# Kernel tuning notes

Hardware: AMD Instinct MI355X
Metric: run time of the kernel (lower is better)

Reference implementation:

```python
import jax, jax.numpy as jnp
import numpy as np

N_NODES = 50000
N_EDGES = 800000
D_IN = 128
HID = 128
N_CLASSES = 2
N_GRAPHS = 500
N_LAYERS = 7


def setup_inputs() -> dict:
    key = jax.random.key(0)
    ks = jax.random.split(key, 8)
    x = jax.random.normal(ks[0], (N_NODES, D_IN), dtype=jnp.float32)
    edge_index = jax.random.randint(ks[1], (2, N_EDGES), 0, N_NODES, dtype=jnp.int32)
    batch = jnp.sort(jax.random.randint(ks[2], (N_NODES,), 0, N_GRAPHS, dtype=jnp.int32))
    s = 1.0 / np.sqrt(HID).astype(np.float32)
    # SAGEConv params: Wl (neighbor lin, with bias bl), Wr (root lin, no bias)
    Wl = jax.random.normal(ks[3], (N_LAYERS, HID, HID), dtype=jnp.float32) * s
    Wr = jax.random.normal(ks[4], (N_LAYERS, HID, HID), dtype=jnp.float32) * s
    bl = jnp.zeros((N_LAYERS, HID), dtype=jnp.float32)
    W_out = jax.random.normal(ks[5], (HID, N_CLASSES), dtype=jnp.float32) * s
    b_out = jnp.zeros((N_CLASSES,), dtype=jnp.float32)
    return {"x": x, "edge_index": edge_index, "batch": batch,
            "Wl": Wl, "Wr": Wr, "bl": bl, "W_out": W_out, "b_out": b_out}


def reference(x, edge_index, batch, Wl, Wr, bl, W_out, b_out):
    n = x.shape[0]
    src, dst = edge_index[0], edge_index[1]  # messages flow src -> dst
    deg = jax.ops.segment_sum(jnp.ones_like(dst, dtype=x.dtype), dst, num_segments=n)
    inv_deg = (1.0 / jnp.clip(deg, 1.0))[:, None]  # [N,1]; zero-degree -> aggregate stays 0

    def sage_layer(h, i):
        # mean aggregation of neighbor features, then linear + root linear
        agg = jax.ops.segment_sum(h[src], dst, num_segments=n) * inv_deg  # [N,H]
        return agg @ Wl[i] + bl[i] + h @ Wr[i]

    h = x
    for i in range(N_LAYERS - 1):
        h = jax.nn.relu(sage_layer(h, i))
    h = sage_layer(h, N_LAYERS - 1)  # last conv: no relu

    pooled = jax.ops.segment_sum(h, batch, num_segments=N_GRAPHS)  # global_add_pool
    # F.dropout with training=False is identity (eval mode)
    return pooled @ W_out + b_out  # [G, num_classes]
```

## Files before the change

### kernel.cpp

```cpp
#include <hip/hip_runtime.h>
#include <stdint.h>

#define NN 50000
#define NE 800000
#define HID 128
#define NG 500
#define NL 7

typedef short bf16x8 __attribute__((ext_vector_type(8)));
typedef float f32x4 __attribute__((ext_vector_type(4)));

__device__ __forceinline__ unsigned short f2bf(float f) {
  unsigned int u = __builtin_bit_cast(unsigned int, f);
  u += 0x7FFFu + ((u >> 16) & 1u);
  return (unsigned short)(u >> 16);
}
__device__ __forceinline__ float bf2f(unsigned short h) {
  unsigned int u = ((unsigned int)h) << 16;
  return __builtin_bit_cast(float, u);
}
__device__ __forceinline__ float bflo(unsigned int u) {
  return __builtin_bit_cast(float, u << 16);
}
__device__ __forceinline__ float bfhi(unsigned int u) {
  return __builtin_bit_cast(float, u & 0xffff0000u);
}

__global__ void k_pre(const float* __restrict__ x, unsigned short* __restrict__ hA,
                      unsigned short* __restrict__ hB,
                      const int* __restrict__ dstE, int* __restrict__ deg,
                      const float* __restrict__ Wl, const float* __restrict__ Wr,
                      unsigned short* __restrict__ wswh,
                      unsigned short* __restrict__ wswl) {
  int i = blockIdx.x * 256 + threadIdx.x;
  if (i < NN * HID / 4) {
    float4 v = ((const float4*)x)[i];
    ushort4 r;
    r.x = f2bf(v.x); r.y = f2bf(v.y); r.z = f2bf(v.z); r.w = f2bf(v.w);
    ((ushort4*)hA)[i] = r;
  }
  if (i < NE) atomicAdd(&deg[dstE[i]], 1);
  if (i < NL * 2 * 4 * 4096) {
    int j = i & 7, ii = (i >> 3) & 15, q = (i >> 7) & 3, t = (i >> 9) & 7;
    int cc = (i >> 12) & 3, m = (i >> 14) & 1, l = i >> 15;
    int k = cc * 32 + q * 8 + j, n = t * 16 + ii;
    const float* W = m ? Wr : Wl;
    float w = W[l * HID * HID + k * HID + n];
    unsigned short hi = f2bf(w);
    unsigned short lo = f2bf(w - bf2f(hi));
    wswh[i] = hi;
    wswl[i] = lo;
  }
  if (i < 2048) {
    int b = i >> 10, r = (i >> 4) & 63, u = i & 15;
    unsigned short* pad = (b ? hB : hA) + (size_t)(NN + r) * HID;
    *(uint4*)&pad[u * 8] = make_uint4(0u, 0u, 0u, 0u);
  }
}

__global__ void k_scan1(const int* __restrict__ deg, int* __restrict__ offs,
                        int* __restrict__ bsum) {
  int i = blockIdx.x * 256 + threadIdx.x;
  int v = (i < NN) ? deg[i] : 0;
  int lane = threadIdx.x & 63, wv = threadIdx.x >> 6;
  int x = v;
  #pragma unroll
  for (int d = 1; d < 64; d <<= 1) {
    int y = __shfl_up(x, d, 64);
    if (lane >= d) x += y;
  }
  __shared__ int wsum[4];
  if (lane == 63) wsum[wv] = x;
  __syncthreads();
  if (threadIdx.x == 0) {
    int s = 0;
    for (int k = 0; k < 4; k++) { int t = wsum[k]; wsum[k] = s; s += t; }
    bsum[blockIdx.x] = s;
  }
  __syncthreads();
  if (i < NN) offs[i] = x - v + wsum[wv];
}

__global__ void k_scan2(int* __restrict__ bsum, int nb) {
  int i = threadIdx.x;
  int v = (i < nb) ? bsum[i] : 0;
  int lane = threadIdx.x & 63, wv = threadIdx.x >> 6;
  int x = v;
  #pragma unroll
  for (int d = 1; d < 64; d <<= 1) {
    int y = __shfl_up(x, d, 64);
    if (lane >= d) x += y;
  }
  __shared__ int wsum[4];
  if (lane == 63) wsum[wv] = x;
  __syncthreads();
  if (threadIdx.x == 0) {
    int s = 0;
    for (int k = 0; k < 4; k++) { int t = wsum[k]; wsum[k] = s; s += t; }
  }
  __syncthreads();
  if (i < nb) bsum[i] = x - v + wsum[wv];
}

__global__ void k_scan3(const int* __restrict__ deg, int* __restrict__ offs,
                        const int* __restrict__ bsum, float* __restrict__ invd) {
  int i = blockIdx.x * 256 + threadIdx.x;
  if (i < NN) {
    offs[i] += bsum[blockIdx.x];
    int d = deg[i];
    invd[i] = 1.0f / (float)(d > 0 ? d : 1);
    if (i == 0) offs[NN] = NE;
  }
}

__global__ void k_fill(const int* __restrict__ src, const int* __restrict__ dst,
                       const int* __restrict__ offs, int* __restrict__ cur,
                       int* __restrict__ csr) {
  int e = blockIdx.x * 256 + threadIdx.x;
  if (e < NE) {
    int d = dst[e];
    int p = atomicAdd(&cur[d], 1);
    csr[offs[d] + p] = src[e];
  }
}

#define ACC8(V) { a0 += bflo(V.x); a1 += bfhi(V.x); a2 += bflo(V.y); \
                  a3 += bfhi(V.y); a4 += bflo(V.z); a5 += bfhi(V.z); \
                  a6 += bflo(V.w); a7 += bfhi(V.w); }

__global__ __launch_bounds__(256, 6) void k_agg(const unsigned short* __restrict__ curh,
                                                const int* __restrict__ offs,
                                                const int* __restrict__ csr,
                                                const float* __restrict__ invd,
                                                unsigned short* __restrict__ agg) {
  const int tid = threadIdx.x;
  const int qw = tid >> 4, sl = tid & 15;
  const int node = blockIdx.x * 16 + qw;
  const unsigned short* rowbase = curh + sl * 8;
  float a0 = 0.f, a1 = 0.f, a2 = 0.f, a3 = 0.f;
  float a4 = 0.f, a5 = 0.f, a6 = 0.f, a7 = 0.f;
  const int s = offs[node], e = offs[node + 1];
  for (int base = s; base < e; base += 16) {
    int idx = (base + sl < e) ? csr[base + sl] : NN;
    uint4 v0 = *(const uint4*)(rowbase + (size_t)__shfl(idx, 0, 16) * HID);
    uint4 v1 = *(const uint4*)(rowbase + (size_t)__shfl(idx, 1, 16) * HID);
    uint4 v2 = *(const uint4*)(rowbase + (size_t)__shfl(idx, 2, 16) * HID);
    uint4 v3 = *(const uint4*)(rowbase + (size_t)__shfl(idx, 3, 16) * HID);
    uint4 v4 = *(const uint4*)(rowbase + (size_t)__shfl(idx, 4, 16) * HID);
    uint4 v5 = *(const uint4*)(rowbase + (size_t)__shfl(idx, 5, 16) * HID);
    uint4 v6 = *(const uint4*)(rowbase + (size_t)__shfl(idx, 6, 16) * HID);
    uint4 v7 = *(const uint4*)(rowbase + (size_t)__shfl(idx, 7, 16) * HID);
    ACC8(v0) ACC8(v1) ACC8(v2) ACC8(v3) ACC8(v4) ACC8(v5) ACC8(v6) ACC8(v7)
    if (base + 8 < e) {
      v0 = *(const uint4*)(rowbase + (size_t)__shfl(idx,  8, 16) * HID);
      v1 = *(const uint4*)(rowbase + (size_t)__shfl(idx,  9, 16) * HID);
      v2 = *(const uint4*)(rowbase + (size_t)__shfl(idx, 10, 16) * HID);
      v3 = *(const uint4*)(rowbase + (size_t)__shfl(idx, 11, 16) * HID);
      v4 = *(const uint4*)(rowbase + (size_t)__shfl(idx, 12, 16) * HID);
      v5 = *(const uint4*)(rowbase + (size_t)__shfl(idx, 13, 16) * HID);
      v6 = *(const uint4*)(rowbase + (size_t)__shfl(idx, 14, 16) * HID);
      v7 = *(const uint4*)(rowbase + (size_t)__shfl(idx, 15, 16) * HID);
      ACC8(v0) ACC8(v1) ACC8(v2) ACC8(v3) ACC8(v4) ACC8(v5) ACC8(v6) ACC8(v7)
    }
  }
  float sc = invd[node];
  a0 *= sc; a1 *= sc; a2 *= sc; a3 *= sc;
  a4 *= sc; a5 *= sc; a6 *= sc; a7 *= sc;
  unsigned int w0 = (unsigned int)f2bf(a0) | ((unsigned int)f2bf(a1) << 16);
  unsigned int w1 = (unsigned int)f2bf(a2) | ((unsigned int)f2bf(a3) << 16);
  unsigned int w2 = (unsigned int)f2bf(a4) | ((unsigned int)f2bf(a5) << 16);
  unsigned int w3 = (unsigned int)f2bf(a6) | ((unsigned int)f2bf(a7) << 16);
  *(uint4*)(agg + (size_t)node * HID + sl * 8) = make_uint4(w0, w1, w2, w3);
}

__global__ __launch_bounds__(256) void k_gemm(const unsigned short* __restrict__ agg,
                                              const unsigned short* __restrict__ curh,
                                              const unsigned short* __restrict__ wswh,
                                              const unsigned short* __restrict__ wswl,
                                              const float* __restrict__ bias,
                                              unsigned short* __restrict__ out,
                                              int relu) {
  __shared__ __align__(16) unsigned short sW2[8192];
  const int tid = threadIdx.x;
  const int lane = tid & 63, wv = tid >> 6;
  const int row0 = blockIdx.x * 64;
  const int mr = (wv << 4) + (lane & 15);
  const int q = lane >> 4;
  const unsigned short* aRow = agg + (size_t)(row0 + mr) * HID + q * 8;
  const unsigned short* hRow = curh + (size_t)(row0 + mr) * HID + q * 8;

  f32x4 acc[8];
  #pragma unroll
  for (int t = 0; t < 8; t++) acc[t] = (f32x4){0.f, 0.f, 0.f, 0.f};

  for (int c = 0; c < 8; ++c) {
    const uint4* wh = (const uint4*)(wswh + c * 4096);
    const uint4* wl = (const uint4*)(wswl + c * 4096);
    ((uint4*)sW2)[tid] = wh[tid];
    ((uint4*)sW2)[tid + 256] = wh[tid + 256];
    ((uint4*)sW2)[tid + 512] = wl[tid];
    ((uint4*)sW2)[tid + 768] = wl[tid + 256];
    __syncthreads();
    bf16x8 a = *(const bf16x8*)(((c < 4) ? aRow : hRow) + (c & 3) * 32);
    #pragma unroll
    for (int t = 0; t < 8; t++) {
      bf16x8 bh = *(const bf16x8*)&sW2[(t * 4 + q) * 128 + (lane & 15) * 8];
      bf16x8 bl2 = *(const bf16x8*)&sW2[4096 + (t * 4 + q) * 128 + (lane & 15) * 8];
      acc[t] = __builtin_amdgcn_mfma_f32_16x16x32_bf16(a, bh, acc[t], 0, 0, 0);
      acc[t] = __builtin_amdgcn_mfma_f32_16x16x32_bf16(a, bl2, acc[t], 0, 0, 0);
    }
    __syncthreads();
  }

  const int ci = lane & 15;
  const int rb = (wv << 4) + (lane >> 4) * 4;
  #pragma unroll
  for (int t = 0; t < 8; t++) {
    int n = t * 16 + ci;
    float bn = bias[n];
    #pragma unroll
    for (int r2 = 0; r2 < 4; r2++) {
      int row = row0 + rb + r2;
      if (row < NN) {
        float v = acc[t][r2] + bn;
        if (relu) v = fmaxf(v, 0.f);
        out[(size_t)row * HID + n] = f2bf(v);
      }
    }
  }
}

__global__ void k_pool(const unsigned short* __restrict__ h,
                       const int* __restrict__ batch, float* __restrict__ pooled) {
  int g = blockIdx.x;
  __shared__ int rng[2];
  __shared__ float tmp[HID];
  if (threadIdx.x < 2) {
    int target = g + threadIdx.x;
    int lo = 0, hi = NN;
    while (lo < hi) {
      int mid = (lo + hi) >> 1;
      if (batch[mid] < target) lo = mid + 1; else hi = mid;
    }
    rng[threadIdx.x] = lo;
  }
  __syncthreads();
  int s = rng[0], e = rng[1];
  int f = threadIdx.x & 127, ro = threadIdx.x >> 7;
  float a = 0.f;
  for (int r = s + ro; r < e; r += 2) a += bf2f(h[(size_t)r * HID + f]);
  if (ro == 1) tmp[f] = a;
  __syncthreads();
  if (ro == 0) pooled[g * HID + f] = a + tmp[f];
}

__global__ void k_out(const float* __restrict__ pooled,
                      const float* __restrict__ Wout,
                      const float* __restrict__ bout,
                      float* __restrict__ out) {
  int g = blockIdx.x;
  int l = threadIdx.x;
  float a = pooled[g * HID + l], b = pooled[g * HID + 64 + l];
  float p0 = a * Wout[l * 2] + b * Wout[(l + 64) * 2];
  float p1 = a * Wout[l * 2 + 1] + b * Wout[(l + 64) * 2 + 1];
  #pragma unroll
  for (int d = 32; d; d >>= 1) {
    p0 += __shfl_down(p0, d, 64);
    p1 += __shfl_down(p1, d, 64);
  }
  if (l == 0) {
    out[g * 2] = p0 + bout[0];
    out[g * 2 + 1] = p1 + bout[1];
  }
}

extern "C" void kernel_launch(void* const* d_in, const int* in_sizes, int n_in,
                              void* d_out, int out_size, void* d_ws, size_t ws_size,
                              hipStream_t stream) {
  const float* x = (const float*)d_in[0];
  const int* ei = (const int*)d_in[1];
  const int* batch = (const int*)d_in[2];
  const float* Wl = (const float*)d_in[3];
  const float* Wr = (const float*)d_in[4];
  const float* bl = (const float*)d_in[5];
  const float* Wout = (const float*)d_in[6];
  const float* bout = (const float*)d_in[7];
  float* out = (float*)d_out;
  const int* srcE = ei;
  const int* dstE = ei + NE;

  char* w = (char*)d_ws;
  unsigned short* hA = (unsigned short*)w;  w += (size_t)(NN + 64) * HID * 2;
  unsigned short* hB = (unsigned short*)w;  w += (size_t)(NN + 64) * HID * 2;
  unsigned short* agg = (unsigned short*)w; w += (size_t)(NN + 64) * HID * 2;
  float* invd = (float*)w;   w += (size_t)NN * 4;
  float* pooled = (float*)w; w += (size_t)NG * HID * 4;
  int* deg = (int*)w;  w += (size_t)NN * 4;
  int* cur = (int*)w;  w += (size_t)NN * 4;
  int* offs = (int*)w; w += (size_t)50004 * 4;
  int* csr = (int*)w;  w += (size_t)NE * 4;
  int* bsum = (int*)w; w += 256 * 4;
  unsigned short* wswh = (unsigned short*)w; w += (size_t)NL * 2 * 4 * 4096 * 2;
  unsigned short* wswl = (unsigned short*)w;

  hipMemsetAsync(deg, 0, (size_t)NN * 2 * 4, stream);
  k_pre<<<(NN * HID / 4 + 255) / 256, 256, 0, stream>>>(x, hA, hB, dstE, deg,
                                                        Wl, Wr, wswh, wswl);
  int nb = (NN + 255) / 256;
  k_scan1<<<nb, 256, 0, stream>>>(deg, offs, bsum);
  k_scan2<<<1, 256, 0, stream>>>(bsum, nb);
  k_scan3<<<nb, 256, 0, stream>>>(deg, offs, bsum, invd);
  k_fill<<<(NE + 255) / 256, 256, 0, stream>>>(srcE, dstE, offs, cur, csr);

  unsigned short* curh = hA;
  unsigned short* nxth = hB;
  for (int l = 0; l < NL; l++) {
    k_agg<<<NN / 16, 256, 0, stream>>>(curh, offs, csr, invd, agg);
    k_gemm<<<(NN + 63) / 64, 256, 0, stream>>>(agg, curh,
                                               wswh + (size_t)l * 2 * 4 * 4096,
                                               wswl + (size_t)l * 2 * 4 * 4096,
                                               bl + l * HID, nxth,
                                               (l < NL - 1) ? 1 : 0);
    unsigned short* t = curh; curh = nxth; nxth = t;
  }
  k_pool<<<NG, 256, 0, stream>>>(curh, batch, pooled);
  k_out<<<NG, 64, 0, stream>>>(pooled, Wout, bout, out);
}
```

Measured before the change: 539.3 us.

## Drop split-bf16 weights, preload full weights to LDS, privatize degree counters

The GEMM stops using a hi/lo bf16 split of the weights and keeps only the rounded high half, which halves the MFMA count. It loads the whole 64KB layer weight block into LDS once per block instead of staging it per chunk behind barriers. Degree counting and CSR fill now use eight privatized counter copies chosen by block index, which reduces atomic contention, and the per-copy scan yields CSR positions directly. The aggregation loop now always issues 16 gathers per iteration, relying on padded zero rows. The trade-offs are lower weight precision in the GEMM and a large LDS footprint that limits occupancy.

```diff
diff --git a/kernel.cpp b/kernel.cpp
--- a/kernel.cpp
+++ b/kernel.cpp
@@ -28,10 +28,9 @@
 
 __global__ void k_pre(const float* __restrict__ x, unsigned short* __restrict__ hA,
                       unsigned short* __restrict__ hB,
-                      const int* __restrict__ dstE, int* __restrict__ deg,
+                      const int* __restrict__ dstE, int* __restrict__ cnt8,
                       const float* __restrict__ Wl, const float* __restrict__ Wr,
-                      unsigned short* __restrict__ wswh,
-                      unsigned short* __restrict__ wswl) {
+                      unsigned short* __restrict__ wswh) {
   int i = blockIdx.x * 256 + threadIdx.x;
   if (i < NN * HID / 4) {
     float4 v = ((const float4*)x)[i];
@@ -39,17 +38,16 @@
     r.x = f2bf(v.x); r.y = f2bf(v.y); r.z = f2bf(v.z); r.w = f2bf(v.w);
     ((ushort4*)hA)[i] = r;
   }
-  if (i < NE) atomicAdd(&deg[dstE[i]], 1);
+  if (i < NE) {
+    int c8 = blockIdx.x & 7;
+    atomicAdd(&cnt8[c8 * NN + dstE[i]], 1);
+  }
   if (i < NL * 2 * 4 * 4096) {
     int j = i & 7, ii = (i >> 3) & 15, q = (i >> 7) & 3, t = (i >> 9) & 7;
     int cc = (i >> 12) & 3, m = (i >> 14) & 1, l = i >> 15;
     int k = cc * 32 + q * 8 + j, n = t * 16 + ii;
     const float* W = m ? Wr : Wl;
-    float w = W[l * HID * HID + k * HID + n];
-    unsigned short hi = f2bf(w);
-    unsigned short lo = f2bf(w - bf2f(hi));
-    wswh[i] = hi;
-    wswl[i] = lo;
+    wswh[i] = f2bf(W[l * HID * HID + k * HID + n]);
   }
   if (i < 2048) {
     int b = i >> 10, r = (i >> 4) & 63, u = i & 15;
@@ -58,10 +56,14 @@
   }
 }
 
-__global__ void k_scan1(const int* __restrict__ deg, int* __restrict__ offs,
+__global__ void k_scan1(const int* __restrict__ cnt8, int* __restrict__ offs,
                         int* __restrict__ bsum) {
   int i = blockIdx.x * 256 + threadIdx.x;
-  int v = (i < NN) ? deg[i] : 0;
+  int v = 0;
+  if (i < NN) {
+    #pragma unroll
+    for (int c = 0; c < 8; ++c) v += cnt8[c * NN + i];
+  }
   int lane = threadIdx.x & 63, wv = threadIdx.x >> 6;
   int x = v;
   #pragma unroll
@@ -102,25 +104,33 @@
   if (i < nb) bsum[i] = x - v + wsum[wv];
 }
 
-__global__ void k_scan3(const int* __restrict__ deg, int* __restrict__ offs,
+__global__ void k_scan3(int* __restrict__ cnt8, int* __restrict__ offs,
                         const int* __restrict__ bsum, float* __restrict__ invd) {
   int i = blockIdx.x * 256 + threadIdx.x;
   if (i < NN) {
-    offs[i] += bsum[blockIdx.x];
-    int d = deg[i];
+    int o = offs[i] + bsum[blockIdx.x];
+    offs[i] = o;
+    int b = o;
+    #pragma unroll
+    for (int c = 0; c < 8; ++c) {
+      int v = cnt8[c * NN + i];
+      cnt8[c * NN + i] = b;
+      b += v;
+    }
+    int d = b - o;
     invd[i] = 1.0f / (float)(d > 0 ? d : 1);
     if (i == 0) offs[NN] = NE;
   }
 }
 
 __global__ void k_fill(const int* __restrict__ src, const int* __restrict__ dst,
-                       const int* __restrict__ offs, int* __restrict__ cur,
-                       int* __restrict__ csr) {
+                       int* __restrict__ cnt8, int* __restrict__ csr) {
   int e = blockIdx.x * 256 + threadIdx.x;
   if (e < NE) {
+    int c8 = blockIdx.x & 7;
     int d = dst[e];
-    int p = atomicAdd(&cur[d], 1);
-    csr[offs[d] + p] = src[e];
+    int p = atomicAdd(&cnt8[c8 * NN + d], 1);
+    csr[p] = src[e];
   }
 }
 
@@ -142,26 +152,24 @@
   const int s = offs[node], e = offs[node + 1];
   for (int base = s; base < e; base += 16) {
     int idx = (base + sl < e) ? csr[base + sl] : NN;
-    uint4 v0 = *(const uint4*)(rowbase + (size_t)__shfl(idx, 0, 16) * HID);
-    uint4 v1 = *(const uint4*)(rowbase + (size_t)__shfl(idx, 1, 16) * HID);
-    uint4 v2 = *(const uint4*)(rowbase + (size_t)__shfl(idx, 2, 16) * HID);
-    uint4 v3 = *(const uint4*)(rowbase + (size_t)__shfl(idx, 3, 16) * HID);
-    uint4 v4 = *(const uint4*)(rowbase + (size_t)__shfl(idx, 4, 16) * HID);
-    uint4 v5 = *(const uint4*)(rowbase + (size_t)__shfl(idx, 5, 16) * HID);
-    uint4 v6 = *(const uint4*)(rowbase + (size_t)__shfl(idx, 6, 16) * HID);
-    uint4 v7 = *(const uint4*)(rowbase + (size_t)__shfl(idx, 7, 16) * HID);
-    ACC8(v0) ACC8(v1) ACC8(v2) ACC8(v3) ACC8(v4) ACC8(v5) ACC8(v6) ACC8(v7)
-    if (base + 8 < e) {
-      v0 = *(const uint4*)(rowbase + (size_t)__shfl(idx,  8, 16) * HID);
-      v1 = *(const uint4*)(rowbase + (size_t)__shfl(idx,  9, 16) * HID);
-      v2 = *(const uint4*)(rowbase + (size_t)__shfl(idx, 10, 16) * HID);
-      v3 = *(const uint4*)(rowbase + (size_t)__shfl(idx, 11, 16) * HID);
-      v4 = *(const uint4*)(rowbase + (size_t)__shfl(idx, 12, 16) * HID);
-      v5 = *(const uint4*)(rowbase + (size_t)__shfl(idx, 13, 16) * HID);
-      v6 = *(const uint4*)(rowbase + (size_t)__shfl(idx, 14, 16) * HID);
-      v7 = *(const uint4*)(rowbase + (size_t)__shfl(idx, 15, 16) * HID);
-      ACC8(v0) ACC8(v1) ACC8(v2) ACC8(v3) ACC8(v4) ACC8(v5) ACC8(v6) ACC8(v7)
-    }
+    uint4 v0  = *(const uint4*)(rowbase + (size_t)__shfl(idx,  0, 16) * HID);
+    uint4 v1  = *(const uint4*)(rowbase + (size_t)__shfl(idx,  1, 16) * HID);
+    uint4 v2  = *(const uint4*)(rowbase + (size_t)__shfl(idx,  2, 16) * HID);
+    uint4 v3  = *(const uint4*)(rowbase + (size_t)__shfl(idx,  3, 16) * HID);
+    uint4 v4  = *(const uint4*)(rowbase + (size_t)__shfl(idx,  4, 16) * HID);
+    uint4 v5  = *(const uint4*)(rowbase + (size_t)__shfl(idx,  5, 16) * HID);
+    uint4 v6  = *(const uint4*)(rowbase + (size_t)__shfl(idx,  6, 16) * HID);
+    uint4 v7  = *(const uint4*)(rowbase + (size_t)__shfl(idx,  7, 16) * HID);
+    uint4 v8  = *(const uint4*)(rowbase + (size_t)__shfl(idx,  8, 16) * HID);
+    uint4 v9  = *(const uint4*)(rowbase + (size_t)__shfl(idx,  9, 16) * HID);
+    uint4 v10 = *(const uint4*)(rowbase + (size_t)__shfl(idx, 10, 16) * HID);
+    uint4 v11 = *(const uint4*)(rowbase + (size_t)__shfl(idx, 11, 16) * HID);
+    uint4 v12 = *(const uint4*)(rowbase + (size_t)__shfl(idx, 12, 16) * HID);
+    uint4 v13 = *(const uint4*)(rowbase + (size_t)__shfl(idx, 13, 16) * HID);
+    uint4 v14 = *(const uint4*)(rowbase + (size_t)__shfl(idx, 14, 16) * HID);
+    uint4 v15 = *(const uint4*)(rowbase + (size_t)__shfl(idx, 15, 16) * HID);
+    ACC8(v0) ACC8(v1) ACC8(v2)  ACC8(v3)  ACC8(v4)  ACC8(v5)  ACC8(v6)  ACC8(v7)
+    ACC8(v8) ACC8(v9) ACC8(v10) ACC8(v11) ACC8(v12) ACC8(v13) ACC8(v14) ACC8(v15)
   }
   float sc = invd[node];
   a0 *= sc; a1 *= sc; a2 *= sc; a3 *= sc;
@@ -176,11 +184,10 @@
 __global__ __launch_bounds__(256) void k_gemm(const unsigned short* __restrict__ agg,
                                               const unsigned short* __restrict__ curh,
                                               const unsigned short* __restrict__ wswh,
-                                              const unsigned short* __restrict__ wswl,
                                               const float* __restrict__ bias,
                                               unsigned short* __restrict__ out,
                                               int relu) {
-  __shared__ __align__(16) unsigned short sW2[8192];
+  __shared__ __align__(16) unsigned short sW[32768];
   const int tid = threadIdx.x;
   const int lane = tid & 63, wv = tid >> 6;
   const int row0 = blockIdx.x * 64;
@@ -189,27 +196,23 @@
   const unsigned short* aRow = agg + (size_t)(row0 + mr) * HID + q * 8;
   const unsigned short* hRow = curh + (size_t)(row0 + mr) * HID + q * 8;
 
+  #pragma unroll
+  for (int it = 0; it < 16; ++it)
+    ((uint4*)sW)[tid + it * 256] = ((const uint4*)wswh)[tid + it * 256];
+  __syncthreads();
+
   f32x4 acc[8];
   #pragma unroll
   for (int t = 0; t < 8; t++) acc[t] = (f32x4){0.f, 0.f, 0.f, 0.f};
 
+  #pragma unroll
   for (int c = 0; c < 8; ++c) {
-    const uint4* wh = (const uint4*)(wswh + c * 4096);
-    const uint4* wl = (const uint4*)(wswl + c * 4096);
-    ((uint4*)sW2)[tid] = wh[tid];
-    ((uint4*)sW2)[tid + 256] = wh[tid + 256];
-    ((uint4*)sW2)[tid + 512] = wl[tid];
-    ((uint4*)sW2)[tid + 768] = wl[tid + 256];
-    __syncthreads();
     bf16x8 a = *(const bf16x8*)(((c < 4) ? aRow : hRow) + (c & 3) * 32);
     #pragma unroll
     for (int t = 0; t < 8; t++) {
-      bf16x8 bh = *(const bf16x8*)&sW2[(t * 4 + q) * 128 + (lane & 15) * 8];
-      bf16x8 bl2 = *(const bf16x8*)&sW2[4096 + (t * 4 + q) * 128 + (lane & 15) * 8];
-      acc[t] = __builtin_amdgcn_mfma_f32_16x16x32_bf16(a, bh, acc[t], 0, 0, 0);
-      acc[t] = __builtin_amdgcn_mfma_f32_16x16x32_bf16(a, bl2, acc[t], 0, 0, 0);
+      bf16x8 b = *(const bf16x8*)&sW[c * 4096 + (t * 4 + q) * 128 + (lane & 15) * 8];
+      acc[t] = __builtin_amdgcn_mfma_f32_16x16x32_bf16(a, b, acc[t], 0, 0, 0);
     }
-    __syncthreads();
   }
 
   const int ci = lane & 15;
@@ -295,22 +298,20 @@
   unsigned short* agg = (unsigned short*)w; w += (size_t)(NN + 64) * HID * 2;
   float* invd = (float*)w;   w += (size_t)NN * 4;
   float* pooled = (float*)w; w += (size_t)NG * HID * 4;
-  int* deg = (int*)w;  w += (size_t)NN * 4;
-  int* cur = (int*)w;  w += (size_t)NN * 4;
+  int* cnt8 = (int*)w; w += (size_t)8 * NN * 4;
   int* offs = (int*)w; w += (size_t)50004 * 4;
   int* csr = (int*)w;  w += (size_t)NE * 4;
   int* bsum = (int*)w; w += 256 * 4;
-  unsigned short* wswh = (unsigned short*)w; w += (size_t)NL * 2 * 4 * 4096 * 2;
-  unsigned short* wswl = (unsigned short*)w;
-
-  hipMemsetAsync(deg, 0, (size_t)NN * 2 * 4, stream);
-  k_pre<<<(NN * HID / 4 + 255) / 256, 256, 0, stream>>>(x, hA, hB, dstE, deg,
-                                                        Wl, Wr, wswh, wswl);
+  unsigned short* wswh = (unsigned short*)w;
+
+  hipMemsetAsync(cnt8, 0, (size_t)8 * NN * 4, stream);
+  k_pre<<<(NN * HID / 4 + 255) / 256, 256, 0, stream>>>(x, hA, hB, dstE, cnt8,
+                                                        Wl, Wr, wswh);
   int nb = (NN + 255) / 256;
-  k_scan1<<<nb, 256, 0, stream>>>(deg, offs, bsum);
+  k_scan1<<<nb, 256, 0, stream>>>(cnt8, offs, bsum);
   k_scan2<<<1, 256, 0, stream>>>(bsum, nb);
-  k_scan3<<<nb, 256, 0, stream>>>(deg, offs, bsum, invd);
-  k_fill<<<(NE + 255) / 256, 256, 0, stream>>>(srcE, dstE, offs, cur, csr);
+  k_scan3<<<nb, 256, 0, stream>>>(cnt8, offs, bsum, invd);
+  k_fill<<<(NE + 255) / 256, 256, 0, stream>>>(srcE, dstE, cnt8, csr);
 
   unsigned short* curh = hA;
   unsigned short* nxth = hB;
@@ -318,7 +319,6 @@
     k_agg<<<NN / 16, 256, 0, stream>>>(curh, offs, csr, invd, agg);
     k_gemm<<<(NN + 63) / 64, 256, 0, stream>>>(agg, curh,
                                                wswh + (size_t)l * 2 * 4 * 4096,
-                                               wswl + (size_t)l * 2 * 4 * 4096,
                                                bl + l * HID, nxth,
                                                (l < NL - 1) ? 1 : 0);
     unsigned short* t = curh; curh = nxth; nxth = t;
```

Result: slower. 558.2 us (+3.5%).
